# Kernel optimization log

Measured on AMD Instinct MI355X. Metric: run time of the kernel, lower is better.

Reference implementation:

```python
import jax, jax.numpy as jnp
import numpy as np

B, S, D = 2, 2048, 2048
H, KVH = 16, 8
HD = D // H          # 128
REP = H // KVH       # 2
FF = 5504
EPS = 1e-5
THETA = 1e6


def rotate_half(x):
    h = x.shape[-1] // 2
    return jnp.concatenate([-x[..., h:], x[..., :h]], axis=-1)


def rms_norm(x, g):
    v = jnp.mean(x.astype(jnp.float32) ** 2, axis=-1, keepdims=True)
    return (x * jax.lax.rsqrt(v + EPS)).astype(x.dtype) * g


def setup_inputs() -> dict:
    key = jax.random.key(0)
    ks = jax.random.split(key, 10)
    # RoPE tables [S, HD]
    inv_freq = 1.0 / (THETA ** (np.arange(0, HD, 2, dtype=np.float32) / HD))
    t = np.arange(S, dtype=np.float32)
    freqs = np.outer(t, inv_freq)                      # [S, HD/2]
    emb = np.concatenate([freqs, freqs], axis=-1)      # [S, HD]
    sc = 0.02
    return {
        "x": jax.random.normal(ks[0], (B, S, D), jnp.float32),
        "cos": jnp.asarray(np.cos(emb)),
        "sin": jnp.asarray(np.sin(emb)),
        "wq": jax.random.normal(ks[1], (H * HD, D), jnp.float32) * sc,
        "wk": jax.random.normal(ks[2], (KVH * HD, D), jnp.float32) * sc,
        "wv": jax.random.normal(ks[3], (KVH * HD, D), jnp.float32) * sc,
        "wo": jax.random.normal(ks[4], (D, H * HD), jnp.float32) * sc,
        "w_gate": jax.random.normal(ks[5], (FF, D), jnp.float32) * sc,
        "w_up": jax.random.normal(ks[6], (FF, D), jnp.float32) * sc,
        "w_down": jax.random.normal(ks[7], (D, FF), jnp.float32) * sc,
        "g1": jnp.ones((D,), jnp.float32),
        "g2": jnp.ones((D,), jnp.float32),
    }


def reference(x, cos, sin, wq, wk, wv, wo, w_gate, w_up, w_down, g1, g2):
    # ---- attention sub-block ----
    h = rms_norm(x, g1)
    q = (h @ wq.T).reshape(B, S, H, HD)
    k = (h @ wk.T).reshape(B, S, KVH, HD)
    v = (h @ wv.T).reshape(B, S, KVH, HD)
    # RoPE: cos/sin [S,HD] -> broadcast over (B, S, heads, HD) via unsqueeze at head dim
    c = cos[:S][:, None, :]
    s = sin[:S][:, None, :]
    q = q * c + rotate_half(q) * s
    k = k * c + rotate_half(k) * s
    # GQA repeat_kv (repeat_interleave on head dim), then bshd -> bhsd
    k = jnp.repeat(k, REP, axis=2).transpose(0, 2, 1, 3)
    v = jnp.repeat(v, REP, axis=2).transpose(0, 2, 1, 3)
    q = q.transpose(0, 2, 1, 3)
    scores = jnp.einsum("bhqd,bhkd->bhqk", q, k) / jnp.sqrt(jnp.float32(HD))
    causal = jnp.triu(jnp.full((S, S), -jnp.inf, jnp.float32), k=1)
    scores = scores + causal[None, None]
    attn = jax.nn.softmax(scores.astype(jnp.float32), axis=-1).astype(scores.dtype)
    out = jnp.einsum("bhqk,bhkd->bhqd", attn, v)
    out = out.transpose(0, 2, 1, 3).reshape(B, S, H * HD)
    x = x + out @ wo.T
    # ---- SwiGLU MLP sub-block ----
    h2 = rms_norm(x, g2)
    mlp = (jax.nn.silu(h2 @ w_gate.T) * (h2 @ w_up.T)) @ w_down.T
    return x + mlp
```

## Files before the change

### kernel.cpp

```cpp
#include <hip/hip_runtime.h>


#define DM 2048
#define SEQ 2048
#define HD 128
#define FF_ 5504
#define QK_SCALE_L2E 0.12751744f

typedef __bf16 bf16x8 __attribute__((ext_vector_type(8)));
typedef float f32x4 __attribute__((ext_vector_type(4)));
typedef float f32x16 __attribute__((ext_vector_type(16)));
typedef unsigned short u16x8 __attribute__((ext_vector_type(8)));
typedef unsigned int u32x4 __attribute__((ext_vector_type(4)));

typedef __attribute__((address_space(1))) void* gas1;
typedef __attribute__((address_space(3))) void* las3;
#define GLDS16(g, s) __builtin_amdgcn_global_load_lds((gas1)(g), (las3)(s), 16, 0, 0)

static __device__ __forceinline__ float bf2f(unsigned short u) {
  union { unsigned int i; float f; } c; c.i = ((unsigned int)u) << 16; return c.f;
}
static __device__ __forceinline__ unsigned short f2bf(float f) {
  __bf16 b = (__bf16)f;
  return __builtin_bit_cast(unsigned short, b);
}
static __device__ __forceinline__ unsigned int pk2(float a, float b) {
  return (unsigned int)f2bf(a) | ((unsigned int)f2bf(b) << 16);
}
static __device__ __forceinline__ float fexp2(float x) { return exp2f(x); }

__global__ __launch_bounds__(256) void k_conv(const float* __restrict__ src,
                                              unsigned short* __restrict__ dst) {
  size_t i = (size_t)(blockIdx.x * 256 + threadIdx.x) * 8;
  float4 a = *(const float4*)&src[i];
  float4 b = *(const float4*)&src[i + 4];
  u16x8 o;
  o[0] = f2bf(a.x); o[1] = f2bf(a.y); o[2] = f2bf(a.z); o[3] = f2bf(a.w);
  o[4] = f2bf(b.x); o[5] = f2bf(b.y); o[6] = f2bf(b.z); o[7] = f2bf(b.w);
  *(u16x8*)&dst[i] = o;
}

__global__ __launch_bounds__(256) void k_conv_gu(const float* __restrict__ g,
                                                 const float* __restrict__ u,
                                                 unsigned short* __restrict__ dst) {
  int i = blockIdx.x * 256 + threadIdx.x;
  int row = i >> 8;
  int c8 = (i & 255) * 8;
  int t = row >> 8, r = row & 255;
  const float* src = (r < 128) ? (g + (size_t)(t * 128 + r) * DM + c8)
                               : (u + (size_t)(t * 128 + (r - 128)) * DM + c8);
  float4 a = *(const float4*)src;
  float4 b = *(const float4*)(src + 4);
  u16x8 o;
  o[0] = f2bf(a.x); o[1] = f2bf(a.y); o[2] = f2bf(a.z); o[3] = f2bf(a.w);
  o[4] = f2bf(b.x); o[5] = f2bf(b.y); o[6] = f2bf(b.z); o[7] = f2bf(b.w);
  *(u16x8*)&dst[(size_t)row * DM + c8] = o;
}

__global__ __launch_bounds__(256) void k_rmsnorm(const float* __restrict__ x,
                                                 const float* __restrict__ g,
                                                 unsigned short* __restrict__ out) {
  int row = blockIdx.x, tid = threadIdx.x;
  const float* xr = x + (size_t)row * DM;
  float4 a = *(const float4*)&xr[tid * 8];
  float4 b = *(const float4*)&xr[tid * 8 + 4];
  float ss = a.x * a.x + a.y * a.y + a.z * a.z + a.w * a.w +
             b.x * b.x + b.y * b.y + b.z * b.z + b.w * b.w;
#pragma unroll
  for (int off = 32; off > 0; off >>= 1) ss += __shfl_xor(ss, off, 64);
  __shared__ float red[4];
  if ((tid & 63) == 0) red[tid >> 6] = ss;
  __syncthreads();
  float rs = rsqrtf((red[0] + red[1] + red[2] + red[3]) * (1.0f / DM) + 1e-5f);
  float4 ga = *(const float4*)&g[tid * 8];
  float4 gb = *(const float4*)&g[tid * 8 + 4];
  u16x8 o;
  o[0] = f2bf(a.x * rs * ga.x); o[1] = f2bf(a.y * rs * ga.y);
  o[2] = f2bf(a.z * rs * ga.z); o[3] = f2bf(a.w * rs * ga.w);
  o[4] = f2bf(b.x * rs * gb.x); o[5] = f2bf(b.y * rs * gb.y);
  o[6] = f2bf(b.z * rs * gb.z); o[7] = f2bf(b.w * rs * gb.w);
  *(u16x8*)&out[(size_t)row * DM + tid * 8] = o;
}

__global__ __launch_bounds__(256) void k_rope(unsigned short* __restrict__ qkv,
                                              const float* __restrict__ cosT,
                                              const float* __restrict__ sinT) {
  int idx = blockIdx.x * 256 + threadIdx.x;
  int j = idx & 63;
  int hh = (idx >> 6) % 24;
  int tok = idx / (64 * 24);
  int s = tok & (SEQ - 1);
  int colbase = (hh < 16) ? hh * HD : DM + (hh - 16) * HD;
  unsigned short* p = qkv + (size_t)tok * 4096 + colbase;
  float lo = bf2f(p[j]), hi = bf2f(p[j + 64]);
  const float* cr = cosT + (size_t)s * HD;
  const float* sr = sinT + (size_t)s * HD;
  float nl = lo * cr[j] - hi * sr[j];
  float nh = hi * cr[j + 64] + lo * sr[j + 64];
  if (hh < 16) { nl *= QK_SCALE_L2E; nh *= QK_SCALE_L2E; }
  p[j] = f2bf(nl);
  p[j + 64] = f2bf(nh);
}

template <int EPI>
__global__ __launch_bounds__(512, 1) void k_gemm8p(
    const unsigned short* __restrict__ A, const unsigned short* __restrict__ Bt,
    unsigned short* __restrict__ outB, float* __restrict__ outF,
    const float* __restrict__ res, int N, int K) {
  __shared__ __attribute__((aligned(16))) unsigned char smem[2][65536];
  const int tid = threadIdx.x, w = tid >> 6, l = tid & 63;
  const int wr = w >> 2, wc = w & 3, lr = l & 15, lg = l >> 4;
  const int nwg = gridDim.x, bid = blockIdx.x;
  const int bswz = (bid & 7) * (nwg >> 3) + (bid >> 3);
  const int mt = bswz & 15, nt = bswz >> 4;
  const int m0 = mt * 256, n0 = nt * 256;
  const int nkt = K >> 6;

  const int rA0 = tid >> 3;
  const int rB0 = ((tid >> 8) << 6) + ((tid >> 3) & 31);
  const int sc = ((tid & 7) ^ ((tid >> 3) & 7)) * 8;
  const unsigned short* Abase = A + (size_t)(m0 + rA0) * K + sc;
  const unsigned short* Bbase = Bt + (size_t)(n0 + rB0) * K + sc;

  auto stA = [&](int kt, int h) {
    unsigned char* dst = smem[kt & 1] + h * 16384;
    const unsigned short* s = Abase + (size_t)(h * 64) * K + kt * 64;
    GLDS16(s, dst + tid * 16);
    GLDS16(s + (size_t)128 * K, dst + (512 + tid) * 16);
  };
  auto stB = [&](int kt, int h) {
    unsigned char* dst = smem[kt & 1] + 32768 + h * 16384;
    const unsigned short* s = Bbase + (size_t)(h * 32) * K + kt * 64;
    GLDS16(s, dst + tid * 16);
    GLDS16(s + (size_t)128 * K, dst + (512 + tid) * 16);
  };

  const int aRow = (wr * 64 + lr) * 128;
  const int bRow = (wc * 32 + lr) * 128;
  const int axr = lr & 7;
#define RDA(BUF, M, KK)                                                        \
  (*(const bf16x8*)((BUF) + ((M) >> 2) * 16384 + aRow + ((M) & 3) * 2048 +     \
                    ((((KK) * 4 + lg) ^ axr) << 4)))
#define RDB(BUF, NN, KK)                                                       \
  (*(const bf16x8*)((BUF) + 32768 + ((NN) >> 1) * 16384 + bRow +               \
                    ((NN) & 1) * 2048 + ((((KK) * 4 + lg) ^ axr) << 4)))

  f32x4 acc[8][4] = {};
  bf16x8 aq[4][2], bq0[2][2], bq1[2][2];

  stA(0, 0); stB(0, 0); stB(0, 1); stA(0, 1);
  asm volatile("s_waitcnt vmcnt(4)" ::: "memory");
  __builtin_amdgcn_s_barrier();

#define MMQ(MB, NB, BQ)                                                        \
  _Pragma("unroll") for (int m = 0; m < 4; m++)                                \
    _Pragma("unroll") for (int n = 0; n < 2; n++)                              \
      _Pragma("unroll") for (int kk = 0; kk < 2; kk++)                         \
          acc[(MB) + m][(NB) + n] = __builtin_amdgcn_mfma_f32_16x16x32_bf16(   \
              aq[m][kk], BQ[n][kk], acc[(MB) + m][(NB) + n], 0, 0, 0);

#define KT8(KT, ST, W1, W2, HASW4)                                             \
  {                                                                            \
    const unsigned char* buf = smem[(KT) & 1];                                 \
                                                        \
    _Pragma("unroll") for (int m = 0; m < 4; m++)                              \
      _Pragma("unroll") for (int kk = 0; kk < 2; kk++)                         \
          aq[m][kk] = RDA(buf, m, kk);                                         \
    _Pragma("unroll") for (int n = 0; n < 2; n++)                              \
      _Pragma("unroll") for (int kk = 0; kk < 2; kk++)                         \
          bq0[n][kk] = RDB(buf, n, kk);                                        \
    if (ST) stA((KT) + 1, 0);                                                  \
    __builtin_amdgcn_s_barrier();                                              \
    asm volatile("s_waitcnt lgkmcnt(0)" ::: "memory");                         \
    __builtin_amdgcn_sched_barrier(0);                                         \
    __builtin_amdgcn_s_setprio(1);                                             \
    MMQ(0, 0, bq0)                                                             \
    __builtin_amdgcn_s_setprio(0);                                             \
    asm volatile("s_waitcnt vmcnt(%0)" ::"i"(W1) : "memory");                  \
    __builtin_amdgcn_s_barrier();                                              \
                                                        \
    _Pragma("unroll") for (int n = 0; n < 2; n++)                              \
      _Pragma("unroll") for (int kk = 0; kk < 2; kk++)                         \
          bq1[n][kk] = RDB(buf, n + 2, kk);                                    \
    if (ST) stB((KT) + 1, 0);                                                  \
    __builtin_amdgcn_s_barrier();                                              \
    asm volatile("s_waitcnt lgkmcnt(0)" ::: "memory");                         \
    __builtin_amdgcn_sched_barrier(0);                                         \
    __builtin_amdgcn_s_setprio(1);                                             \
    MMQ(0, 2, bq1)                                                             \
    __builtin_amdgcn_s_setprio(0);                                             \
    asm volatile("s_waitcnt vmcnt(%0)" ::"i"(W2) : "memory");                  \
    __builtin_amdgcn_s_barrier();                                              \
                                                        \
    _Pragma("unroll") for (int m = 0; m < 4; m++)                              \
      _Pragma("unroll") for (int kk = 0; kk < 2; kk++)                         \
          aq[m][kk] = RDA(buf, m + 4, kk);                                     \
    if (ST) stB((KT) + 1, 1);                                                  \
    __builtin_amdgcn_s_barrier();                                              \
    asm volatile("s_waitcnt lgkmcnt(0)" ::: "memory");                         \
    __builtin_amdgcn_sched_barrier(0);                                         \
    __builtin_amdgcn_s_setprio(1);                                             \
    MMQ(4, 2, bq1)                                                             \
    __builtin_amdgcn_s_setprio(0);                                             \
    __builtin_amdgcn_s_barrier();                                              \
                                                        \
    if (ST) stA((KT) + 1, 1);                                                  \
    __builtin_amdgcn_s_barrier();                                              \
    __builtin_amdgcn_s_setprio(1);                                             \
    MMQ(4, 0, bq0)                                                             \
    __builtin_amdgcn_s_setprio(0);                                             \
    if (HASW4) asm volatile("s_waitcnt vmcnt(4)" ::: "memory");                \
    __builtin_amdgcn_s_barrier();                                              \
  }

  for (int kt = 0; kt < nkt - 1; kt++) KT8(kt, true, 4, 4, true);
  KT8(nkt - 1, false, 2, 0, false);
#undef KT8
#undef MMQ
#undef RDA
#undef RDB

  const int rbase = wr * 128 + lg * 4;
  const int cbase = wc * 64 + lr;
  if constexpr (EPI == 0) {
#pragma unroll
    for (int m = 0; m < 8; m++)
#pragma unroll
      for (int n = 0; n < 4; n++)
#pragma unroll
        for (int j = 0; j < 4; j++)
          outB[(size_t)(m0 + rbase + m * 16 + j) * N + n0 + cbase + n * 16] =
              f2bf(acc[m][n][j]);
  } else if constexpr (EPI == 1) {
#pragma unroll
    for (int m = 0; m < 8; m++)
#pragma unroll
      for (int n = 0; n < 4; n++)
#pragma unroll
        for (int j = 0; j < 4; j++) {
          size_t o = (size_t)(m0 + rbase + m * 16 + j) * N + n0 + cbase + n * 16;
          outF[o] = res[o] + acc[m][n][j];
        }
  } else {
    float* gl = (float*)smem;
    const int ab = n0 >> 1;
    __syncthreads();
#pragma unroll
    for (int half = 0; half < 2; half++) {
      if (wr == half && wc < 2) {
#pragma unroll
        for (int m = 0; m < 8; m++)
#pragma unroll
          for (int n = 0; n < 4; n++)
#pragma unroll
            for (int j = 0; j < 4; j++)
              gl[(m * 16 + lg * 4 + j) * 128 + wc * 64 + n * 16 + lr] = acc[m][n][j];
      }
      __syncthreads();
      if (wr == half && wc >= 2) {
#pragma unroll
        for (int m = 0; m < 8; m++)
#pragma unroll
          for (int n = 0; n < 4; n++)
#pragma unroll
            for (int j = 0; j < 4; j++) {
              int rl = m * 16 + lg * 4 + j;
              int cl = (wc - 2) * 64 + n * 16 + lr;
              float g = gl[rl * 128 + cl];
              float s = g / (1.0f + __expf(-g));
              outB[(size_t)(m0 + half * 128 + rl) * FF_ + ab + cl] = f2bf(s * acc[m][n][j]);
            }
      }
      __syncthreads();
    }
  }
}

template <int BN, int EPI, int PIPE>
__global__ __launch_bounds__(512, 2) void k_gemm8(
    const unsigned short* __restrict__ A, const unsigned short* __restrict__ Bt,
    unsigned short* __restrict__ outB, float* __restrict__ outF,
    const float* __restrict__ res, int N, int K) {
  constexpr int NF = BN / 64;
  constexpr int BSTMT = BN / 128;
  constexpr int ABY = 256 * 64;
  constexpr int BBY = BN * 64;
  constexpr int BUF = ABY + BBY;
  constexpr int VPK = 2 + BSTMT;
  __shared__ __attribute__((aligned(16))) unsigned char smem[4 * BUF];

  const int tid = threadIdx.x, w = tid >> 6, l = tid & 63;
  const int wr = w >> 2, wc = w & 3, lr = l & 15, lg = l >> 4;
  const int nwg = gridDim.x, bid = blockIdx.x;
  const int bswz = (bid & 7) * (nwg >> 3) + (bid >> 3);
  const int mt = bswz & 15, nt = bswz >> 4;
  const int m0 = mt * 256, n0 = nt * BN;
  const int nk = K >> 5;

  const int srow = w * 16 + (l >> 2);
  const int sg8 = ((l & 3) ^ ((l >> 3) & 3)) * 8;
  const unsigned short* Asrc = A + (size_t)(m0 + srow) * K + sg8;
  const unsigned short* Bsrc = Bt + (size_t)(n0 + srow) * K + sg8;
  const int aoff = (wr * 128 + lr) * 64 + ((lg ^ ((lr >> 1) & 3)) << 4);
  const int boff = (wc * (BN / 4) + lr) * 64 + ((lg ^ ((lr >> 1) & 3)) << 4);

  auto stageA = [&](int kt) {
    unsigned char* bb = smem + (kt & 3) * BUF;
#pragma unroll
    for (int i = 0; i < 2; i++)
      GLDS16(Asrc + (size_t)i * 128 * K + kt * 32, bb + (i * 512 + w * 64) * 16);
  };
  auto stageB = [&](int kt) {
    unsigned char* bb = smem + (kt & 3) * BUF + ABY;
#pragma unroll
    for (int i = 0; i < BSTMT; i++)
      GLDS16(Bsrc + (size_t)i * 128 * K + kt * 32, bb + (i * 512 + w * 64) * 16);
  };

  f32x4 acc[8][NF] = {};

  for (int kt = 0; kt < 3; kt++) { stageA(kt); stageB(kt); }
  asm volatile("s_waitcnt vmcnt(%0)" ::"i"(2 * VPK) : "memory");
  __builtin_amdgcn_s_barrier();
  for (int kt = 0; kt < nk; kt++) {
    unsigned char* ba = smem + (kt & 3) * BUF;
    unsigned char* bb = ba + ABY;
    const bool st = (kt + 3) < nk;
    bf16x8 am[8], bnf[NF];
#pragma unroll
    for (int m = 0; m < 8; m++) am[m] = *(const bf16x8*)(ba + aoff + m * 1024);
#pragma unroll
    for (int n = 0; n < NF; n++) bnf[n] = *(const bf16x8*)(bb + boff + n * 1024);
    if (st) { stageA(kt + 3); stageB(kt + 3); }
    __builtin_amdgcn_s_barrier();
    __builtin_amdgcn_s_setprio(1);
#pragma unroll
    for (int m = 0; m < 8; m++)
#pragma unroll
      for (int n = 0; n < NF; n++)
        acc[m][n] = __builtin_amdgcn_mfma_f32_16x16x32_bf16(am[m], bnf[n], acc[m][n], 0, 0, 0);
    __builtin_amdgcn_s_setprio(0);
    if (kt <= nk - 4)      asm volatile("s_waitcnt vmcnt(%0)" ::"i"(2 * VPK) : "memory");
    else if (kt == nk - 3) asm volatile("s_waitcnt vmcnt(%0)" ::"i"(VPK) : "memory");
    else if (kt == nk - 2) asm volatile("s_waitcnt vmcnt(0)" ::: "memory");
    __builtin_amdgcn_s_barrier();
  }

  const int rbase = wr * 128 + lg * 4;
  const int cbase = wc * (BN / 4) + lr;
  if constexpr (EPI == 0) {
#pragma unroll
    for (int m = 0; m < 8; m++)
#pragma unroll
      for (int n = 0; n < NF; n++)
#pragma unroll
        for (int j = 0; j < 4; j++)
          outB[(size_t)(m0 + rbase + m * 16 + j) * N + n0 + cbase + n * 16] =
              f2bf(acc[m][n][j]);
  } else {
#pragma unroll
    for (int m = 0; m < 8; m++)
#pragma unroll
      for (int n = 0; n < NF; n++)
#pragma unroll
        for (int j = 0; j < 4; j++) {
          size_t o = (size_t)(m0 + rbase + m * 16 + j) * N + n0 + cbase + n * 16;
          outF[o] = res[o] + acc[m][n][j];
        }
  }
}

__global__ __launch_bounds__(256) void k_attn2(const unsigned short* __restrict__ qkv,
                                               unsigned short* __restrict__ out) {
  __shared__ __attribute__((aligned(16))) unsigned short lK[2][64 * 128];
  __shared__ __attribute__((aligned(16))) unsigned short lV[2][128 * 64];
  const float NEG = -3.0e38f;
  int bx = blockIdx.x;
  int qtile = 15 - (bx >> 5);
  int hb = bx & 31;
  int h = hb & 15, b = hb >> 4;
  int q0 = qtile * 128;
  int tid = threadIdx.x, w = tid >> 6, l = tid & 63;
  int l31 = l & 31, half2 = l >> 5;
  const unsigned short* base = qkv + (size_t)b * SEQ * 4096;
  const unsigned short* Kp = base + 2048 + (h >> 1) * HD;
  const unsigned short* Vp = base + 3072 + (h >> 1) * HD;
  const int qw = q0 + w * 32;

  bf16x8 qf[8];
  {
    const unsigned short* qrow = base + (size_t)(qw + l31) * 4096 + h * HD + half2 * 8;
#pragma unroll
    for (int d = 0; d < 8; d++) qf[d] = *(const bf16x8*)(qrow + d * 16);
  }

  f32x16 oacc[4] = {};
  float mrow = NEG, lsum = 0.0f;

  const int vp = tid & 31, vdc = tid >> 5;
  u16x8 va0, va1, vb0, vb1;

  auto stageK = [&](int t) {
    unsigned char* dst = (unsigned char*)lK[t & 1];
#pragma unroll
    for (int i = 0; i < 4; i++) {
      int c = i * 256 + tid;
      int row = c >> 4;
      int g = (c & 15) ^ (row & 7);
      GLDS16(Kp + (size_t)(t * 64 + row) * 4096 + g * 8, dst + (i * 256 + w * 64) * 16);
    }
  };
  auto loadV = [&](int t) {
    const unsigned short* vr = Vp + (size_t)(t * 64 + vp * 2) * 4096 + vdc * 16;
    va0 = *(const u16x8*)(vr);
    va1 = *(const u16x8*)(vr + 8);
    vb0 = *(const u16x8*)(vr + 4096);
    vb1 = *(const u16x8*)(vr + 4096 + 8);
  };

  const int nt = (q0 >> 6) + 2;
  stageK(0);
  loadV(0);

  for (int t = 0; t < nt; t++) {
    __syncthreads();
    {
      unsigned char* lv = (unsigned char*)lV[t & 1];
#pragma unroll
      for (int j = 0; j < 16; j++) {
        int dd = vdc * 16 + j;
        unsigned short lo = (j < 8) ? va0[j] : va1[j - 8];
        unsigned short hi = (j < 8) ? vb0[j] : vb1[j - 8];
        unsigned int pkv = (unsigned int)lo | ((unsigned int)hi << 16);
        *(unsigned int*)(lv + dd * 128 + (((vp >> 2) ^ (dd & 7)) * 16) + (vp & 3) * 4) = pkv;
      }
    }
    __syncthreads();
    if (t + 1 < nt) { stageK(t + 1); loadV(t + 1); }
    const int kv0 = t * 64;
    if (kv0 <= qw + 31) {
      f32x16 sc[2] = {};
      const unsigned char* lk = (const unsigned char*)lK[t & 1];
#pragma unroll
      for (int hh = 0; hh < 2; hh++) {
        int kk = hh * 32 + l31;
        const unsigned char* krow = lk + kk * 256;
#pragma unroll
        for (int d = 0; d < 8; d++) {
          bf16x8 kf = *(const bf16x8*)(krow + (((d * 2 + half2) ^ (kk & 7)) * 16));
          sc[hh] = __builtin_amdgcn_mfma_f32_32x32x16_bf16(kf, qf[d], sc[hh], 0, 0, 0);
        }
      }
      const int qa = qw + l31;
      if (kv0 + 63 > qw) {
#pragma unroll
        for (int hh = 0; hh < 2; hh++)
#pragma unroll
          for (int r = 0; r < 16; r++) {
            int kva = kv0 + hh * 32 + (r & 3) + 8 * (r >> 2) + 4 * half2;
            if (kva > qa) sc[hh][r] = NEG;
          }
      }
      float mx = sc[0][0];
#pragma unroll
      for (int r = 1; r < 16; r++) mx = fmaxf(mx, sc[0][r]);
#pragma unroll
      for (int r = 0; r < 16; r++) mx = fmaxf(mx, sc[1][r]);
      mx = fmaxf(mx, __shfl_xor(mx, 32));
      bool ok = (mx <= mrow + 11.0f);
      if (__ballot(ok) != ~0ull) {
        float mnew = fmaxf(mrow, mx);
        float fct = fexp2(mrow - mnew);
        mrow = mnew;
        lsum *= fct;
#pragma unroll
        for (int r = 0; r < 16; r++) {
          int rr = (r & 3) + 8 * (r >> 2) + 4 * half2;
          float fr = __shfl(fct, rr);
#pragma unroll
          for (int d = 0; d < 4; d++) oacc[d][r] *= fr;
        }
      }
      float ps = 0.0f;
#pragma unroll
      for (int hh = 0; hh < 2; hh++)
#pragma unroll
        for (int r = 0; r < 16; r++) {
          float e = fexp2(sc[hh][r] - mrow);
          sc[hh][r] = e;
          ps += e;
        }
      ps += __shfl_xor(ps, 32);
      lsum += ps;
      const unsigned char* lv = (const unsigned char*)lV[t & 1];
#pragma unroll
      for (int s = 0; s < 4; s++) {
        const int hh = s >> 1;
        const int r0 = (s & 1) * 8;
        unsigned int lo0, lo1, hi0, hi1;
        if (hh == 0) {
          lo0 = pk2(sc[0][r0 + 0], sc[0][r0 + 1]); lo1 = pk2(sc[0][r0 + 2], sc[0][r0 + 3]);
          hi0 = pk2(sc[0][r0 + 4], sc[0][r0 + 5]); hi1 = pk2(sc[0][r0 + 6], sc[0][r0 + 7]);
        } else {
          lo0 = pk2(sc[1][r0 + 0], sc[1][r0 + 1]); lo1 = pk2(sc[1][r0 + 2], sc[1][r0 + 3]);
          hi0 = pk2(sc[1][r0 + 4], sc[1][r0 + 5]); hi1 = pk2(sc[1][r0 + 6], sc[1][r0 + 7]);
        }
        unsigned int s0 = half2 ? lo0 : hi0, s1 = half2 ? lo1 : hi1;
        unsigned int rc0 = (unsigned int)__shfl_xor((int)s0, 32);
        unsigned int rc1 = (unsigned int)__shfl_xor((int)s1, 32);
        u32x4 fr;
        fr[0] = half2 ? rc0 : lo0; fr[1] = half2 ? rc1 : lo1;
        fr[2] = half2 ? hi0 : rc0; fr[3] = half2 ? hi1 : rc1;
        bf16x8 pa = __builtin_bit_cast(bf16x8, fr);
#pragma unroll
        for (int d = 0; d < 4; d++) {
          int dd = d * 32 + l31;
          bf16x8 vf = *(const bf16x8*)(lv + dd * 128 + (((s * 2 + half2) ^ (dd & 7)) * 16));
          oacc[d] = __builtin_amdgcn_mfma_f32_32x32x16_bf16(pa, vf, oacc[d], 0, 0, 0);
        }
      }
    }
  }
  float inv = 1.0f / lsum;
#pragma unroll
  for (int r = 0; r < 16; r++) {
    int rr = (r & 3) + 8 * (r >> 2) + 4 * half2;
    float ir = __shfl(inv, rr);
    size_t ob = ((size_t)(b * SEQ + qw + rr)) * 2048 + h * HD;
#pragma unroll
    for (int d = 0; d < 4; d++)
      out[ob + d * 32 + l31] = f2bf(oacc[d][r] * ir);
  }
}

extern "C" void kernel_launch(void* const* d_in, const int* in_sizes, int n_in,
                              void* d_out, int out_size, void* d_ws, size_t ws_size,
                              hipStream_t stream) {
  const float* x = (const float*)d_in[0];
  const float* cosT = (const float*)d_in[1];
  const float* sinT = (const float*)d_in[2];
  const float* wq = (const float*)d_in[3];
  const float* wk = (const float*)d_in[4];
  const float* wv = (const float*)d_in[5];
  const float* wo = (const float*)d_in[6];
  const float* wg = (const float*)d_in[7];
  const float* wu = (const float*)d_in[8];
  const float* wd = (const float*)d_in[9];
  const float* g1 = (const float*)d_in[10];
  const float* g2 = (const float*)d_in[11];
  float* out = (float*)d_out;
  char* ws = (char*)d_ws;

  unsigned short* wqkv = (unsigned short*)(ws + 0);
  unsigned short* hbuf = (unsigned short*)(ws + 16777216);
  unsigned short* qkv = (unsigned short*)(ws + 33554432);
  unsigned short* attn_o = (unsigned short*)(ws + 67108864);
  unsigned short* wo_bf = (unsigned short*)(ws + 83886080);
  unsigned short* wgu = (unsigned short*)(ws + 33554432);
  unsigned short* act = (unsigned short*)(ws + 92274688);
  unsigned short* wdown = (unsigned short*)(ws + 0);

  k_conv<<<2048, 256, 0, stream>>>(wq, wqkv);
  k_conv<<<1024, 256, 0, stream>>>(wk, wqkv + 4194304);
  k_conv<<<1024, 256, 0, stream>>>(wv, wqkv + 6291456);
  k_rmsnorm<<<4096, 256, 0, stream>>>(x, g1, hbuf);
  k_gemm8p<0><<<256, 512, 0, stream>>>(hbuf, wqkv, qkv, nullptr, nullptr,
                                       4096, 2048);
  k_rope<<<24576, 256, 0, stream>>>(qkv, cosT, sinT);
  k_attn2<<<512, 256, 0, stream>>>(qkv, attn_o);
  k_conv<<<2048, 256, 0, stream>>>(wo, wo_bf);
  k_gemm8<128, 1, 0><<<256, 512, 0, stream>>>(attn_o, wo_bf, nullptr, out, x,
                                              2048, 2048);
  k_rmsnorm<<<4096, 256, 0, stream>>>(out, g2, hbuf);
  k_conv_gu<<<11008, 256, 0, stream>>>(wg, wu, wgu);
  k_gemm8p<2><<<688, 512, 0, stream>>>(hbuf, wgu, act, nullptr, nullptr,
                                       11008, 2048);
  k_conv<<<5504, 256, 0, stream>>>(wd, wdown);
  k_gemm8<128, 1, 0><<<256, 512, 0, stream>>>(act, wdown, nullptr, out, out,
                                              2048, 5504);
}
```

Before: 595.7 us.

## Fuse RoPE into QKV GEMM epilogue and merge weight conversions into one kernel

Removes the standalone RoPE kernel by applying the rotation and the Q scale in a new GEMM epilogue (EPI 3). The epilogue exchanges each lane's partner half through shared memory, then reads cos and sin from global memory. The four wq/wk/wv/wo conversion launches become one k_convW launch, and the block-index swizzle is removed from both GEMMs. The fused epilogue adds syncthreads and scattered stores, and dropping the swizzle may reduce L2 locality.

```diff
diff --git a/kernel.cpp b/kernel.cpp
--- a/kernel.cpp
+++ b/kernel.cpp
@@ -28,6 +28,28 @@
   return (unsigned int)f2bf(a) | ((unsigned int)f2bf(b) << 16);
 }
 static __device__ __forceinline__ float fexp2(float x) { return exp2f(x); }
+
+__global__ __launch_bounds__(256) void k_convW(const float* __restrict__ wq,
+                                               const float* __restrict__ wk,
+                                               const float* __restrict__ wv,
+                                               const float* __restrict__ wo,
+                                               unsigned short* __restrict__ wqkv,
+                                               unsigned short* __restrict__ wo_bf) {
+  int b = blockIdx.x;
+  const float* src;
+  unsigned short* dst;
+  if (b < 2048)      { src = wq + (size_t)b * DM;            dst = wqkv + (size_t)b * DM; }
+  else if (b < 3072) { src = wk + (size_t)(b - 2048) * DM;   dst = wqkv + 4194304 + (size_t)(b - 2048) * DM; }
+  else if (b < 4096) { src = wv + (size_t)(b - 3072) * DM;   dst = wqkv + 6291456 + (size_t)(b - 3072) * DM; }
+  else               { src = wo + (size_t)(b - 4096) * DM;   dst = wo_bf + (size_t)(b - 4096) * DM; }
+  int i = threadIdx.x * 8;
+  float4 a = *(const float4*)&src[i];
+  float4 c = *(const float4*)&src[i + 4];
+  u16x8 o;
+  o[0] = f2bf(a.x); o[1] = f2bf(a.y); o[2] = f2bf(a.z); o[3] = f2bf(a.w);
+  o[4] = f2bf(c.x); o[5] = f2bf(c.y); o[6] = f2bf(c.z); o[7] = f2bf(c.w);
+  *(u16x8*)&dst[i] = o;
+}
 
 __global__ __launch_bounds__(256) void k_conv(const float* __restrict__ src,
                                               unsigned short* __restrict__ dst) {
@@ -82,36 +104,16 @@
   *(u16x8*)&out[(size_t)row * DM + tid * 8] = o;
 }
 
-__global__ __launch_bounds__(256) void k_rope(unsigned short* __restrict__ qkv,
-                                              const float* __restrict__ cosT,
-                                              const float* __restrict__ sinT) {
-  int idx = blockIdx.x * 256 + threadIdx.x;
-  int j = idx & 63;
-  int hh = (idx >> 6) % 24;
-  int tok = idx / (64 * 24);
-  int s = tok & (SEQ - 1);
-  int colbase = (hh < 16) ? hh * HD : DM + (hh - 16) * HD;
-  unsigned short* p = qkv + (size_t)tok * 4096 + colbase;
-  float lo = bf2f(p[j]), hi = bf2f(p[j + 64]);
-  const float* cr = cosT + (size_t)s * HD;
-  const float* sr = sinT + (size_t)s * HD;
-  float nl = lo * cr[j] - hi * sr[j];
-  float nh = hi * cr[j + 64] + lo * sr[j + 64];
-  if (hh < 16) { nl *= QK_SCALE_L2E; nh *= QK_SCALE_L2E; }
-  p[j] = f2bf(nl);
-  p[j + 64] = f2bf(nh);
-}
-
 template <int EPI>
 __global__ __launch_bounds__(512, 1) void k_gemm8p(
     const unsigned short* __restrict__ A, const unsigned short* __restrict__ Bt,
     unsigned short* __restrict__ outB, float* __restrict__ outF,
-    const float* __restrict__ res, int N, int K) {
+    const float* __restrict__ res, int N, int K,
+    const float* __restrict__ cosT, const float* __restrict__ sinT) {
   __shared__ __attribute__((aligned(16))) unsigned char smem[2][65536];
   const int tid = threadIdx.x, w = tid >> 6, l = tid & 63;
   const int wr = w >> 2, wc = w & 3, lr = l & 15, lg = l >> 4;
-  const int nwg = gridDim.x, bid = blockIdx.x;
-  const int bswz = (bid & 7) * (nwg >> 3) + (bid >> 3);
+  const int bswz = blockIdx.x;
   const int mt = bswz & 15, nt = bswz >> 4;
   const int m0 = mt * 256, n0 = nt * 256;
   const int nkt = K >> 6;
@@ -241,7 +243,7 @@
           size_t o = (size_t)(m0 + rbase + m * 16 + j) * N + n0 + cbase + n * 16;
           outF[o] = res[o] + acc[m][n][j];
         }
-  } else {
+  } else if constexpr (EPI == 2) {
     float* gl = (float*)smem;
     const int ab = n0 >> 1;
     __syncthreads();
@@ -273,10 +275,48 @@
       }
       __syncthreads();
     }
+  } else {
+    if (nt >= 12) {
+#pragma unroll
+      for (int m = 0; m < 8; m++)
+#pragma unroll
+        for (int n = 0; n < 4; n++)
+#pragma unroll
+          for (int j = 0; j < 4; j++)
+            outB[(size_t)(m0 + rbase + m * 16 + j) * N + n0 + cbase + n * 16] =
+                f2bf(acc[m][n][j]);
+    } else {
+      float* gl = (float*)smem;
+      const float qs = (nt < 8) ? QK_SCALE_L2E : 1.0f;
+      __syncthreads();
+      for (int m = 0; m < 8; m++) {
+#pragma unroll
+        for (int n = 0; n < 4; n++)
+#pragma unroll
+          for (int j = 0; j < 4; j++)
+            gl[wr * 4096 + (lg * 4 + j) * 256 + wc * 64 + n * 16 + lr] = acc[m][n][j];
+        __syncthreads();
+#pragma unroll
+        for (int n = 0; n < 4; n++)
+#pragma unroll
+          for (int j = 0; j < 4; j++) {
+            int c = wc * 64 + n * 16 + lr;
+            int d = c & 127;
+            int row = m0 + wr * 128 + m * 16 + lg * 4 + j;
+            int s = row & (SEQ - 1);
+            float own = acc[m][n][j];
+            float prt = gl[wr * 4096 + (lg * 4 + j) * 256 + (c ^ 64)];
+            float cv = cosT[s * HD + d], sv = sinT[s * HD + d];
+            float rot = own * cv + ((d & 64) ? prt : -prt) * sv;
+            outB[(size_t)row * N + n0 + c] = f2bf(rot * qs);
+          }
+        __syncthreads();
+      }
+    }
   }
 }
 
-template <int BN, int EPI, int PIPE>
+template <int BN, int EPI>
 __global__ __launch_bounds__(512, 2) void k_gemm8(
     const unsigned short* __restrict__ A, const unsigned short* __restrict__ Bt,
     unsigned short* __restrict__ outB, float* __restrict__ outF,
@@ -291,8 +331,7 @@
 
   const int tid = threadIdx.x, w = tid >> 6, l = tid & 63;
   const int wr = w >> 2, wc = w & 3, lr = l & 15, lg = l >> 4;
-  const int nwg = gridDim.x, bid = blockIdx.x;
-  const int bswz = (bid & 7) * (nwg >> 3) + (bid >> 3);
+  const int bswz = blockIdx.x;
   const int mt = bswz & 15, nt = bswz >> 4;
   const int m0 = mt * 256, n0 = nt * BN;
   const int nk = K >> 5;
@@ -560,22 +599,18 @@
   unsigned short* act = (unsigned short*)(ws + 92274688);
   unsigned short* wdown = (unsigned short*)(ws + 0);
 
-  k_conv<<<2048, 256, 0, stream>>>(wq, wqkv);
-  k_conv<<<1024, 256, 0, stream>>>(wk, wqkv + 4194304);
-  k_conv<<<1024, 256, 0, stream>>>(wv, wqkv + 6291456);
+  k_convW<<<6144, 256, 0, stream>>>(wq, wk, wv, wo, wqkv, wo_bf);
   k_rmsnorm<<<4096, 256, 0, stream>>>(x, g1, hbuf);
-  k_gemm8p<0><<<256, 512, 0, stream>>>(hbuf, wqkv, qkv, nullptr, nullptr,
-                                       4096, 2048);
-  k_rope<<<24576, 256, 0, stream>>>(qkv, cosT, sinT);
+  k_gemm8p<3><<<256, 512, 0, stream>>>(hbuf, wqkv, qkv, nullptr, nullptr,
+                                       4096, 2048, cosT, sinT);
   k_attn2<<<512, 256, 0, stream>>>(qkv, attn_o);
-  k_conv<<<2048, 256, 0, stream>>>(wo, wo_bf);
-  k_gemm8<128, 1, 0><<<256, 512, 0, stream>>>(attn_o, wo_bf, nullptr, out, x,
-                                              2048, 2048);
+  k_gemm8<128, 1><<<256, 512, 0, stream>>>(attn_o, wo_bf, nullptr, out, x,
+                                           2048, 2048);
   k_rmsnorm<<<4096, 256, 0, stream>>>(out, g2, hbuf);
   k_conv_gu<<<11008, 256, 0, stream>>>(wg, wu, wgu);
   k_gemm8p<2><<<688, 512, 0, stream>>>(hbuf, wgu, act, nullptr, nullptr,
-                                       11008, 2048);
+                                       11008, 2048, nullptr, nullptr);
   k_conv<<<5504, 256, 0, stream>>>(wd, wdown);
-  k_gemm8<128, 1, 0><<<256, 512, 0, stream>>>(act, wdown, nullptr, out, out,
-                                              2048, 5504);
-}
+  k_gemm8<128, 1><<<256, 512, 0, stream>>>(act, wdown, nullptr, out, out,
+                                           2048, 5504);
+}
```

New measurement: 584.4 us. No clear change (-1.9%).
